# Optimization experiments

Measured on AMD Instinct MI355X. Metric: run time of the kernel, lower is better.

Reference implementation:

```python
import jax, jax.numpy as jnp
import numpy as np

D_MODEL = 2048
D_HEAD = 64
Q_HEADS = 32
KV_HEADS = 8


def rope(x):
    # x: [B, S, H, D], rotate interleaved pairs along last dim
    B, S, H, D = x.shape
    pos = jnp.arange(S, dtype=x.dtype)
    freq = 1.0 / (10000.0 ** (jnp.arange(0, D, 2, dtype=x.dtype) / D))  # [D/2]
    theta = pos[:, None] * freq[None, :]                                 # [S, D/2]
    cos = jnp.cos(theta)[None, :, None, :]
    sin = jnp.sin(theta)[None, :, None, :]
    xr = x.reshape(B, S, H, D // 2, 2)
    x1, x2 = xr[..., 0], xr[..., 1]
    out = jnp.stack((x1 * cos - x2 * sin, x1 * sin + x2 * cos), axis=-1)
    return out.reshape(B, S, H, D)


def setup_inputs() -> dict:
    key = jax.random.key(0)
    ks = jax.random.split(key, 7)
    x = jax.random.normal(ks[0], (1, 2048, D_MODEL), dtype=jnp.float32)
    W_q = jax.random.normal(ks[1], (Q_HEADS * D_HEAD, D_MODEL), dtype=jnp.float32) * 0.02
    b_q = jnp.zeros((Q_HEADS * D_HEAD,), dtype=jnp.float32)
    W_kv = jax.random.normal(ks[2], (2 * KV_HEADS * D_HEAD, D_MODEL), dtype=jnp.float32) * 0.02
    b_kv = jnp.zeros((2 * KV_HEADS * D_HEAD,), dtype=jnp.float32)
    W_out = jax.random.normal(ks[3], (D_MODEL, D_MODEL), dtype=jnp.float32) * 0.02
    b_out = jnp.zeros((D_MODEL,), dtype=jnp.float32)
    return {"x": x, "W_q": W_q, "b_q": b_q, "W_kv": W_kv, "b_kv": b_kv,
            "W_out": W_out, "b_out": b_out}


def reference(x, W_q, b_q, W_kv, b_kv, W_out, b_out):
    B, S, _ = x.shape
    g = Q_HEADS // KV_HEADS
    Q = (x @ W_q.T + b_q).reshape(B, S, Q_HEADS, D_HEAD)
    kv = x @ W_kv.T + b_kv
    K, V = jnp.split(kv, 2, axis=-1)
    K = K.reshape(B, S, KV_HEADS, D_HEAD)
    V = V.reshape(B, S, KV_HEADS, D_HEAD)
    Q = rope(Q)
    K = rope(K)
    K = jnp.repeat(K, g, axis=2)  # [B, S, Q_HEADS, D_HEAD]
    V = jnp.repeat(V, g, axis=2)
    scale = 1.0 / (D_HEAD ** 0.5)
    scores = jnp.einsum('bqhd,bkhd->bhqk', Q, K) * scale  # [B,H,S,S]
    # note: original calls non-inplace masked_fill and discards it, so no causal mask applied
    probs = jax.nn.softmax(scores, axis=-1)
    attn = jnp.einsum('bhqk,bkhd->bqhd', probs, V).reshape(B, S, D_MODEL)
    return attn @ W_out.T + b_out
```

## Files before the change

kernel.cpp:

```cpp
#include <hip/hip_runtime.h>
#include <hip/hip_bf16.h>
#include <math.h>

#define S_LEN 2048
#define D_MODEL 2048
#define Q_HEADS 32
#define KV_HEADS 8

typedef __attribute__((ext_vector_type(8))) short short8;
typedef __attribute__((ext_vector_type(4))) float f32x4;

__device__ __forceinline__ short bf16_rne(float f) {
  unsigned u = __float_as_uint(f);
  unsigned r = (u + 0x7FFFu + ((u >> 16) & 1u)) >> 16;
  return (short)r;
}
__device__ __forceinline__ void dma16(const short* g, short* l) {
  __builtin_amdgcn_global_load_lds(
      (const __attribute__((address_space(1))) void*)g,
      (__attribute__((address_space(3))) void*)l, 16, 0, 0);
}
__device__ __forceinline__ void fast_sincos(float theta, float& sn, float& cs) {
  double rev = (double)theta * 0.15915494309189535;
  float fr = (float)(rev - floor(rev));
  sn = __builtin_amdgcn_sinf(fr);
  cs = __builtin_amdgcn_cosf(fr);
}
__device__ __forceinline__ void cvt8(const float* src, short* dst, int i) {
  float4 a = *(const float4*)&src[i];
  float4 b = *(const float4*)&src[i + 4];
  short8 h;
  h[0] = bf16_rne(a.x); h[1] = bf16_rne(a.y);
  h[2] = bf16_rne(a.z); h[3] = bf16_rne(a.w);
  h[4] = bf16_rne(b.x); h[5] = bf16_rne(b.y);
  h[6] = bf16_rne(b.z); h[7] = bf16_rne(b.w);
  *(short8*)&dst[i] = h;
}

#define NM (2048 * 2048)
#define NKV (1024 * 2048)

__global__ __launch_bounds__(256) void cvt_all(
    const float* __restrict__ x,    short* __restrict__ xh,
    const float* __restrict__ wq,   short* __restrict__ wqh,
    const float* __restrict__ wkv,  short* __restrict__ wkvh,
    const float* __restrict__ wo,   short* __restrict__ woh) {
  int i = (blockIdx.x * 256 + threadIdx.x) * 8;
  if (i < NM) { cvt8(x, xh, i); return; }
  i -= NM;
  if (i < NM) { cvt8(wq, wqh, i); return; }
  i -= NM;
  if (i < NKV) { cvt8(wkv, wkvh, i); return; }
  i -= NKV;
  cvt8(wo, woh, i);
}

__global__ __launch_bounds__(256) void gemm_nt1_dual(
    const short* __restrict__ Ah,
    const short* __restrict__ Bq, const short* __restrict__ Bkv,
    const float* __restrict__ bq, const float* __restrict__ bkv,
    float* __restrict__ Cq, float* __restrict__ Ckv,
    int Nq, int Nkv, int K) {
  __shared__ short As[2][128 * 32];
  __shared__ short Bs[2][128 * 32];
  const int tid = threadIdx.x;
  const int w = tid >> 6, lane = tid & 63;
  const int l16 = lane & 15, quad = lane >> 4;
  const int bm = blockIdx.y * 128;
  const int bnG = blockIdx.x * 128;

  const short* Bsrc; const float* bias; float* Cp; int pitch; int bn;
  if (bnG < Nq) { Bsrc = Bq;  bias = bq;  Cp = Cq;  pitch = Nq;  bn = bnG; }
  else          { Bsrc = Bkv; bias = bkv; Cp = Ckv; pitch = Nkv; bn = bnG - Nq; }

  const int drow0 = w * 16 + (lane >> 2);
  const int drow1 = drow0 + 64;
  const int slot = lane & 3;
  const int ch0 = slot ^ ((drow0 >> 1) & 3);
  const int ch1 = slot ^ ((drow1 >> 1) & 3);
  const short* gA0 = &Ah[(size_t)(bm + drow0) * K + ch0 * 8];
  const short* gA1 = &Ah[(size_t)(bm + drow1) * K + ch1 * 8];
  const short* gB0 = &Bsrc[(size_t)(bn + drow0) * K + ch0 * 8];
  const short* gB1 = &Bsrc[(size_t)(bn + drow1) * K + ch1 * 8];
  const int dA0 = (w * 16) * 32, dA1 = (64 + w * 16) * 32;

  const int wm = (w & 1) * 64, wn = (w >> 1) * 64;
  int offA[4], offB[4];
#pragma unroll
  for (int i = 0; i < 4; ++i) {
    int R = wm + i * 16 + l16;
    offA[i] = R * 32 + (quad ^ ((R >> 1) & 3)) * 8;
    int Rb = wn + i * 16 + l16;
    offB[i] = Rb * 32 + (quad ^ ((Rb >> 1) & 3)) * 8;
  }

  f32x4 acc[4][4];
#pragma unroll
  for (int i = 0; i < 4; ++i)
#pragma unroll
    for (int j = 0; j < 4; ++j)
#pragma unroll
      for (int e = 0; e < 4; ++e) acc[i][j][e] = 0.f;

  const int T = K / 32;
  dma16(gA0, &As[0][dA0]);
  dma16(gA1, &As[0][dA1]);
  dma16(gB0, &Bs[0][dA0]);
  dma16(gB1, &Bs[0][dA1]);
  __syncthreads();

  for (int t = 0; t < T; ++t) {
    const int cur = t & 1, nxt = cur ^ 1;
    if (t + 1 < T) {
      const int ko = (t + 1) * 32;
      dma16(gA0 + ko, &As[nxt][dA0]);
      dma16(gA1 + ko, &As[nxt][dA1]);
      dma16(gB0 + ko, &Bs[nxt][dA0]);
      dma16(gB1 + ko, &Bs[nxt][dA1]);
    }
    short8 af[4], bf[4];
#pragma unroll
    for (int i = 0; i < 4; ++i) af[i] = *(const short8*)&As[cur][offA[i]];
#pragma unroll
    for (int j = 0; j < 4; ++j) bf[j] = *(const short8*)&Bs[cur][offB[j]];
#pragma unroll
    for (int i = 0; i < 4; ++i)
#pragma unroll
      for (int j = 0; j < 4; ++j)
        acc[i][j] = __builtin_amdgcn_mfma_f32_16x16x32_bf16(af[i], bf[j], acc[i][j], 0, 0, 0);
    __syncthreads();
  }

#pragma unroll
  for (int i = 0; i < 4; ++i) {
#pragma unroll
    for (int j = 0; j < 4; ++j) {
      const int col = bn + wn + j * 16 + l16;
      const float bv = bias[col];
      const int row0 = bm + wm + i * 16 + quad * 4;
#pragma unroll
      for (int e = 0; e < 4; ++e)
        Cp[(size_t)(row0 + e) * pitch + col] = acc[i][j][e] + bv;
    }
  }
}

__global__ __launch_bounds__(256) void gemm_nt1s(
    const short* __restrict__ A, const short* __restrict__ B,
    const float* __restrict__ bias, float* __restrict__ C,
    int N, int K) {
  __shared__ short As[2][128 * 32];
  __shared__ short Bs[2][64 * 32];
  const int tid = threadIdx.x;
  const int w = tid >> 6, lane = tid & 63;
  const int l16 = lane & 15, quad = lane >> 4;
  const int bm = blockIdx.y * 128;
  const int bn = blockIdx.x * 64;

  const int drow0 = w * 16 + (lane >> 2);
  const int drow1 = drow0 + 64;
  const int slot = lane & 3;
  const int ch0 = slot ^ ((drow0 >> 1) & 3);
  const int ch1 = slot ^ ((drow1 >> 1) & 3);
  const size_t a0 = (size_t)(bm + drow0) * K + ch0 * 8;
  const size_t a1 = (size_t)(bm + drow1) * K + ch1 * 8;
  const size_t b0 = (size_t)(bn + drow0) * K + ch0 * 8;
  const int dA0 = (w * 16) * 32, dA1 = (64 + w * 16) * 32;

  const int wm = (w & 1) * 64, wn = (w >> 1) * 32;
  int offA[4], offB[2];
#pragma unroll
  for (int i = 0; i < 4; ++i) {
    int R = wm + i * 16 + l16;
    offA[i] = R * 32 + (quad ^ ((R >> 1) & 3)) * 8;
  }
#pragma unroll
  for (int j = 0; j < 2; ++j) {
    int R = wn + j * 16 + l16;
    offB[j] = R * 32 + (quad ^ ((R >> 1) & 3)) * 8;
  }

  f32x4 acc[4][2];
#pragma unroll
  for (int i = 0; i < 4; ++i)
#pragma unroll
    for (int j = 0; j < 2; ++j)
#pragma unroll
      for (int e = 0; e < 4; ++e) acc[i][j][e] = 0.f;

  const int T = K / 32;
  dma16(A + a0, &As[0][dA0]);
  dma16(A + a1, &As[0][dA1]);
  dma16(B + b0, &Bs[0][dA0]);
  __syncthreads();

  for (int t = 0; t < T; ++t) {
    const int cur = t & 1, nxt = cur ^ 1;
    if (t + 1 < T) {
      const int ko = (t + 1) * 32;
      dma16(A + a0 + ko, &As[nxt][dA0]);
      dma16(A + a1 + ko, &As[nxt][dA1]);
      dma16(B + b0 + ko, &Bs[nxt][dA0]);
    }
    short8 af[4], bf[2];
#pragma unroll
    for (int i = 0; i < 4; ++i) af[i] = *(const short8*)&As[cur][offA[i]];
#pragma unroll
    for (int j = 0; j < 2; ++j) bf[j] = *(const short8*)&Bs[cur][offB[j]];
#pragma unroll
    for (int i = 0; i < 4; ++i)
#pragma unroll
      for (int j = 0; j < 2; ++j)
        acc[i][j] = __builtin_amdgcn_mfma_f32_16x16x32_bf16(af[i], bf[j], acc[i][j], 0, 0, 0);
    __syncthreads();
  }

#pragma unroll
  for (int i = 0; i < 4; ++i) {
#pragma unroll
    for (int j = 0; j < 2; ++j) {
      const int col = bn + wn + j * 16 + l16;
      const float bv = bias[col];
      const int row0 = bm + wm + i * 16 + quad * 4;
#pragma unroll
      for (int e = 0; e < 4; ++e)
        C[(size_t)(row0 + e) * N + col] = acc[i][j][e] + bv;
    }
  }
}

#define QSCALE 0.18033688011112042f

__global__ __launch_bounds__(256) void rope_q_pack(
    const float* __restrict__ Qf, short* __restrict__ Qb) {
  const int g = blockIdx.x * 256 + threadIdx.x;
  const int s = g >> 10;
  const int rem = g & 1023;
  const int h = rem >> 5, j = rem & 31;
  const double e = (2.0 * j) / 64.0;
  const float freq = (float)pow(10000.0, -e);
  const float theta = (float)s * freq;
  float sn, cs;
  fast_sincos(theta, sn, cs);
  const float* p = &Qf[(size_t)s * D_MODEL + h * 64 + 2 * j];
  const float x1 = p[0], x2 = p[1];
  short2 o;
  o.x = bf16_rne((x1 * cs - x2 * sn) * QSCALE);
  o.y = bf16_rne((x1 * sn + x2 * cs) * QSCALE);
  *(short2*)&Qb[((size_t)h * S_LEN + s) * 64 + 2 * j] = o;
}

__global__ __launch_bounds__(256) void rope_kv_pack(
    const float* __restrict__ KVf, short* __restrict__ Kb,
    short* __restrict__ Vt) {
  const int st = blockIdx.x, kvh = blockIdx.y;
  const int tid = threadIdx.x;
  __shared__ short Vtile[64][72];

  {
    const int sr = tid >> 2, sc = (tid & 3) * 16;
    const int s = st * 64 + sr;
    const float* kg = &KVf[(size_t)s * 1024 + kvh * 64 + sc];
    short tmp[16];
#pragma unroll
    for (int i = 0; i < 8; ++i) {
      const int j = (sc >> 1) + i;
      const double e = (2.0 * j) / 64.0;
      const float freq = (float)pow(10000.0, -e);
      const float theta = (float)s * freq;
      float sn, cs;
      fast_sincos(theta, sn, cs);
      const float x1 = kg[2 * i], x2 = kg[2 * i + 1];
      tmp[2 * i]     = bf16_rne(x1 * cs - x2 * sn);
      tmp[2 * i + 1] = bf16_rne(x1 * sn + x2 * cs);
    }
    short* out = &Kb[((size_t)kvh * S_LEN + s) * 64 + sc];
    *(short8*)&out[0] = *(short8*)&tmp[0];
    *(short8*)&out[8] = *(short8*)&tmp[8];
  }

  {
    const int sr = tid >> 2, sc = (tid & 3) * 16;
    const float* vg = &KVf[(size_t)(st * 64 + sr) * 1024 + 512 + kvh * 64 + sc];
    short tmp[16];
#pragma unroll
    for (int c = 0; c < 16; c += 4) {
      float4 v = *(const float4*)&vg[c];
      tmp[c + 0] = bf16_rne(v.x);
      tmp[c + 1] = bf16_rne(v.y);
      tmp[c + 2] = bf16_rne(v.z);
      tmp[c + 3] = bf16_rne(v.w);
    }
    *(short8*)&Vtile[sr][sc]     = *(short8*)&tmp[0];
    *(short8*)&Vtile[sr][sc + 8] = *(short8*)&tmp[8];
  }
  __syncthreads();
  {
    const int d = tid & 63, kchunk = tid >> 6;
    short tmp[16];
#pragma unroll
    for (int k = 0; k < 16; ++k) tmp[k] = Vtile[kchunk * 16 + k][d];
    short* out = &Vt[((size_t)kvh * 64 + d) * S_LEN + st * 64 + kchunk * 16];
    *(short8*)&out[0] = *(short8*)&tmp[0];
    *(short8*)&out[8] = *(short8*)&tmp[8];
  }
}

__global__ __launch_bounds__(256) void flash6(
    const short* __restrict__ Qb, const short* __restrict__ Kb,
    const short* __restrict__ Vt, short* __restrict__ Oh) {
  const int qt = blockIdx.x, h = blockIdx.y;
  const int kvh = h >> 2;
  const int tid = threadIdx.x;
  const int w = tid >> 6, lane = tid & 63;
  const int l16 = lane & 15, quad = lane >> 4;

  __shared__ short Ks[2][64 * 64];
  __shared__ short Vs[2][64 * 64];
  __shared__ short Ps[64 * 72];

  const short* Kh = Kb + (size_t)kvh * S_LEN * 64;
  const short* Vh = Vt + (size_t)kvh * 64 * S_LEN;
  const int qr = qt * 64 + w * 16 + l16;

  short8 qf0 = *(const short8*)&Qb[((size_t)h * S_LEN + qr) * 64 + quad * 8];
  short8 qf1 = *(const short8*)&Qb[((size_t)h * S_LEN + qr) * 64 + 32 + quad * 8];

  short8 ones;
#pragma unroll
  for (int e = 0; e < 8; ++e) ones[e] = (short)0x3F80;

  const int drow = lane >> 3;
  const int ch = (lane & 7) ^ drow;
  const short* gK = &Kh[(size_t)(w * 16 + drow) * 64 + ch * 8];
  const short* gV = &Vh[(size_t)(w * 16 + drow) * S_LEN + ch * 8];

  const int sl0 = quad ^ (l16 & 7);
  int offT[4][2];
#pragma unroll
  for (int m = 0; m < 4; ++m) {
    offT[m][0] = (m * 16 + l16) * 64 + sl0 * 8;
    offT[m][1] = (m * 16 + l16) * 64 + (sl0 ^ 4) * 8;
  }
  const int prow = (w * 16 + l16) * 72;

  f32x4 accl;
#pragma unroll
  for (int e = 0; e < 4; ++e) accl[e] = 0.f;
  f32x4 acco[4];
#pragma unroll
  for (int m = 0; m < 4; ++m)
#pragma unroll
    for (int e = 0; e < 4; ++e) acco[m][e] = 0.f;

  dma16(gK,               &Ks[0][(w * 16) * 64]);
  dma16(gK + 8 * 64,      &Ks[0][(w * 16 + 8) * 64]);
  dma16(gV,               &Vs[0][(w * 16) * 64]);
  dma16(gV + 8 * S_LEN,   &Vs[0][(w * 16 + 8) * 64]);
  __syncthreads();

  for (int t = 0; t < 32; ++t) {
    const int cur = t & 1, nxt = cur ^ 1;
    if (t + 1 < 32) {
      const short* gKn = gK + (t + 1) * 4096;
      const short* gVn = gV + (t + 1) * 64;
      dma16(gKn,             &Ks[nxt][(w * 16) * 64]);
      dma16(gKn + 8 * 64,    &Ks[nxt][(w * 16 + 8) * 64]);
      dma16(gVn,             &Vs[nxt][(w * 16) * 64]);
      dma16(gVn + 8 * S_LEN, &Vs[nxt][(w * 16 + 8) * 64]);
    }

    const short* kc = Ks[cur];
    f32x4 accs[4];
#pragma unroll
    for (int m = 0; m < 4; ++m)
#pragma unroll
      for (int e = 0; e < 4; ++e) accs[m][e] = 0.f;
#pragma unroll
    for (int m = 0; m < 4; ++m) {
      short8 k0 = *(const short8*)&kc[offT[m][0]];
      short8 k1 = *(const short8*)&kc[offT[m][1]];
      accs[m] = __builtin_amdgcn_mfma_f32_16x16x32_bf16(k0, qf0, accs[m], 0, 0, 0);
      accs[m] = __builtin_amdgcn_mfma_f32_16x16x32_bf16(k1, qf1, accs[m], 0, 0, 0);
    }

#pragma unroll
    for (int m = 0; m < 4; ++m) {
      float p0 = exp2f(accs[m][0]);
      float p1 = exp2f(accs[m][1]);
      float p2 = exp2f(accs[m][2]);
      float p3 = exp2f(accs[m][3]);
      unsigned u01 = __builtin_amdgcn_perm(__float_as_uint(p1), __float_as_uint(p0), 0x07060302u);
      unsigned u23 = __builtin_amdgcn_perm(__float_as_uint(p3), __float_as_uint(p2), 0x07060302u);
      *(uint2*)&Ps[prow + m * 16 + quad * 4] = make_uint2(u01, u23);
    }

    short8 pf0 = *(const short8*)&Ps[prow + quad * 8];
    short8 pf1 = *(const short8*)&Ps[prow + 32 + quad * 8];
    accl = __builtin_amdgcn_mfma_f32_16x16x32_bf16(ones, pf0, accl, 0, 0, 0);
    accl = __builtin_amdgcn_mfma_f32_16x16x32_bf16(ones, pf1, accl, 0, 0, 0);
    const short* vc = Vs[cur];
#pragma unroll
    for (int m = 0; m < 4; ++m) {
      short8 v0 = *(const short8*)&vc[offT[m][0]];
      short8 v1 = *(const short8*)&vc[offT[m][1]];
      acco[m] = __builtin_amdgcn_mfma_f32_16x16x32_bf16(v0, pf0, acco[m], 0, 0, 0);
      acco[m] = __builtin_amdgcn_mfma_f32_16x16x32_bf16(v1, pf1, acco[m], 0, 0, 0);
    }

    __syncthreads();
  }

  const float inv = 1.f / accl[0];
#pragma unroll
  for (int m = 0; m < 4; ++m) {
    short4 h4;
    h4.x = bf16_rne(acco[m][0] * inv);
    h4.y = bf16_rne(acco[m][1] * inv);
    h4.z = bf16_rne(acco[m][2] * inv);
    h4.w = bf16_rne(acco[m][3] * inv);
    const size_t base = (size_t)qr * D_MODEL + h * 64 + m * 16 + quad * 4;
    *(short4*)&Oh[base] = h4;
  }
}

extern "C" void kernel_launch(void* const* d_in, const int* in_sizes, int n_in,
                              void* d_out, int out_size, void* d_ws, size_t ws_size,
                              hipStream_t stream) {
  const float* x     = (const float*)d_in[0];
  const float* W_q   = (const float*)d_in[1];
  const float* b_q   = (const float*)d_in[2];
  const float* W_kv  = (const float*)d_in[3];
  const float* b_kv  = (const float*)d_in[4];
  const float* W_out = (const float*)d_in[5];
  const float* b_out = (const float*)d_in[6];
  float* out = (float*)d_out;

  char* ws = (char*)d_ws;
  float* Qbuf  = (float*)(ws);
  float* KVbuf = (float*)(ws + (16u << 20));
  short* xh    = (short*)(ws + (24u << 20));
  short* Wqh   = (short*)(ws + (32u << 20));
  short* Wkvh  = (short*)(ws + (40u << 20));
  short* Woh   = (short*)(ws + (44u << 20));
  short* Qb    = (short*)(ws + (52u << 20));
  short* Kb    = (short*)(ws + (60u << 20));
  short* Vtb   = (short*)(ws + (62u << 20));
  short* Ath   = xh;

  cvt_all<<<7168, 256, 0, stream>>>(x, xh, W_q, Wqh, W_kv, Wkvh, W_out, Woh);

  gemm_nt1_dual<<<dim3(3072 / 128, 2048 / 128), 256, 0, stream>>>(
      xh, Wqh, Wkvh, b_q, b_kv, Qbuf, KVbuf, 2048, 1024, 2048);

  rope_q_pack<<<(S_LEN * 1024) / 256, 256, 0, stream>>>(Qbuf, Qb);
  rope_kv_pack<<<dim3(S_LEN / 64, KV_HEADS), 256, 0, stream>>>(KVbuf, Kb, Vtb);

  flash6<<<dim3(S_LEN / 64, Q_HEADS), 256, 0, stream>>>(Qb, Kb, Vtb, Ath);

  gemm_nt1s<<<dim3(2048 / 64, 2048 / 128), 256, 0, stream>>>(
      Ath, Woh, b_out, out, 2048, 2048);
}
```

Measured before the change: 279.3 us.

## Load V fragments directly into registers in flash kernel; enlarge output GEMM tile

The attention kernel stops staging V through shared memory. Each wave now reads its V fragments straight from global memory into registers and prefetches the next tile after the PV MFMAs, which drops the V LDS buffers and cuts shared-memory use, and launch bounds now ask for four blocks per CU. The output projection GEMM moves from a 128x64 to a 128x128 tile so each block reuses the A tile across more columns, at the cost of fewer blocks (256) and more accumulator registers. Each wave redundantly loading the full V tile from global/L2 adds global traffic.

```diff
diff --git a/kernel.cpp b/kernel.cpp
--- a/kernel.cpp
+++ b/kernel.cpp
@@ -145,72 +145,72 @@
   }
 }
 
-__global__ __launch_bounds__(256) void gemm_nt1s(
+__global__ __launch_bounds__(256) void gemm_nt1_big(
     const short* __restrict__ A, const short* __restrict__ B,
     const float* __restrict__ bias, float* __restrict__ C,
     int N, int K) {
   __shared__ short As[2][128 * 32];
-  __shared__ short Bs[2][64 * 32];
+  __shared__ short Bs[2][128 * 32];
   const int tid = threadIdx.x;
   const int w = tid >> 6, lane = tid & 63;
   const int l16 = lane & 15, quad = lane >> 4;
   const int bm = blockIdx.y * 128;
-  const int bn = blockIdx.x * 64;
+  const int bn = blockIdx.x * 128;
 
   const int drow0 = w * 16 + (lane >> 2);
   const int drow1 = drow0 + 64;
   const int slot = lane & 3;
   const int ch0 = slot ^ ((drow0 >> 1) & 3);
   const int ch1 = slot ^ ((drow1 >> 1) & 3);
-  const size_t a0 = (size_t)(bm + drow0) * K + ch0 * 8;
-  const size_t a1 = (size_t)(bm + drow1) * K + ch1 * 8;
-  const size_t b0 = (size_t)(bn + drow0) * K + ch0 * 8;
+  const short* gA0 = &A[(size_t)(bm + drow0) * K + ch0 * 8];
+  const short* gA1 = &A[(size_t)(bm + drow1) * K + ch1 * 8];
+  const short* gB0 = &B[(size_t)(bn + drow0) * K + ch0 * 8];
+  const short* gB1 = &B[(size_t)(bn + drow1) * K + ch1 * 8];
   const int dA0 = (w * 16) * 32, dA1 = (64 + w * 16) * 32;
 
-  const int wm = (w & 1) * 64, wn = (w >> 1) * 32;
-  int offA[4], offB[2];
+  const int wm = (w & 1) * 64, wn = (w >> 1) * 64;
+  int offA[4], offB[4];
 #pragma unroll
   for (int i = 0; i < 4; ++i) {
     int R = wm + i * 16 + l16;
     offA[i] = R * 32 + (quad ^ ((R >> 1) & 3)) * 8;
-  }
-#pragma unroll
-  for (int j = 0; j < 2; ++j) {
-    int R = wn + j * 16 + l16;
-    offB[j] = R * 32 + (quad ^ ((R >> 1) & 3)) * 8;
-  }
-
-  f32x4 acc[4][2];
+    int Rb = wn + i * 16 + l16;
+    offB[i] = Rb * 32 + (quad ^ ((Rb >> 1) & 3)) * 8;
+  }
+
+  f32x4 acc[4][4];
 #pragma unroll
   for (int i = 0; i < 4; ++i)
 #pragma unroll
-    for (int j = 0; j < 2; ++j)
+    for (int j = 0; j < 4; ++j)
 #pragma unroll
       for (int e = 0; e < 4; ++e) acc[i][j][e] = 0.f;
 
   const int T = K / 32;
-  dma16(A + a0, &As[0][dA0]);
-  dma16(A + a1, &As[0][dA1]);
-  dma16(B + b0, &Bs[0][dA0]);
+  dma16(gA0, &As[0][dA0]);
+  dma16(gA1, &As[0][dA1]);
+  dma16(gB0, &Bs[0][dA0]);
+  dma16(gB1, &Bs[0][dA1]);
   __syncthreads();
 
   for (int t = 0; t < T; ++t) {
     const int cur = t & 1, nxt = cur ^ 1;
     if (t + 1 < T) {
       const int ko = (t + 1) * 32;
-      dma16(A + a0 + ko, &As[nxt][dA0]);
-      dma16(A + a1 + ko, &As[nxt][dA1]);
-      dma16(B + b0 + ko, &Bs[nxt][dA0]);
-    }
-    short8 af[4], bf[2];
+      dma16(gA0 + ko, &As[nxt][dA0]);
+      dma16(gA1 + ko, &As[nxt][dA1]);
+      dma16(gB0 + ko, &Bs[nxt][dA0]);
+      dma16(gB1 + ko, &Bs[nxt][dA1]);
+    }
+    short8 af[4], bf[4];
 #pragma unroll
     for (int i = 0; i < 4; ++i) af[i] = *(const short8*)&As[cur][offA[i]];
 #pragma unroll
-    for (int j = 0; j < 2; ++j) bf[j] = *(const short8*)&Bs[cur][offB[j]];
+    for (int j = 0; j < 4; ++j) bf[j] = *(const short8*)&Bs[cur][offB[j]];
 #pragma unroll
     for (int i = 0; i < 4; ++i)
 #pragma unroll
-      for (int j = 0; j < 2; ++j)
+      for (int j = 0; j < 4; ++j)
         acc[i][j] = __builtin_amdgcn_mfma_f32_16x16x32_bf16(af[i], bf[j], acc[i][j], 0, 0, 0);
     __syncthreads();
   }
@@ -218,7 +218,7 @@
 #pragma unroll
   for (int i = 0; i < 4; ++i) {
 #pragma unroll
-    for (int j = 0; j < 2; ++j) {
+    for (int j = 0; j < 4; ++j) {
       const int col = bn + wn + j * 16 + l16;
       const float bv = bias[col];
       const int row0 = bm + wm + i * 16 + quad * 4;
@@ -306,7 +306,7 @@
   }
 }
 
-__global__ __launch_bounds__(256) void flash6(
+__global__ __launch_bounds__(256, 4) void flash7(
     const short* __restrict__ Qb, const short* __restrict__ Kb,
     const short* __restrict__ Vt, short* __restrict__ Oh) {
   const int qt = blockIdx.x, h = blockIdx.y;
@@ -316,7 +316,6 @@
   const int l16 = lane & 15, quad = lane >> 4;
 
   __shared__ short Ks[2][64 * 64];
-  __shared__ short Vs[2][64 * 64];
   __shared__ short Ps[64 * 72];
 
   const short* Kh = Kb + (size_t)kvh * S_LEN * 64;
@@ -333,7 +332,6 @@
   const int drow = lane >> 3;
   const int ch = (lane & 7) ^ drow;
   const short* gK = &Kh[(size_t)(w * 16 + drow) * 64 + ch * 8];
-  const short* gV = &Vh[(size_t)(w * 16 + drow) * S_LEN + ch * 8];
 
   const int sl0 = quad ^ (l16 & 7);
   int offT[4][2];
@@ -344,6 +342,11 @@
   }
   const int prow = (w * 16 + l16) * 72;
 
+  const short* gV[4];
+#pragma unroll
+  for (int m = 0; m < 4; ++m)
+    gV[m] = &Vh[(size_t)(m * 16 + l16) * S_LEN + quad * 8];
+
   f32x4 accl;
 #pragma unroll
   for (int e = 0; e < 4; ++e) accl[e] = 0.f;
@@ -353,21 +356,22 @@
 #pragma unroll
     for (int e = 0; e < 4; ++e) acco[m][e] = 0.f;
 
-  dma16(gK,               &Ks[0][(w * 16) * 64]);
-  dma16(gK + 8 * 64,      &Ks[0][(w * 16 + 8) * 64]);
-  dma16(gV,               &Vs[0][(w * 16) * 64]);
-  dma16(gV + 8 * S_LEN,   &Vs[0][(w * 16 + 8) * 64]);
+  dma16(gK,          &Ks[0][(w * 16) * 64]);
+  dma16(gK + 8 * 64, &Ks[0][(w * 16 + 8) * 64]);
+  short8 vf[4][2];
+#pragma unroll
+  for (int m = 0; m < 4; ++m) {
+    vf[m][0] = *(const short8*)(gV[m]);
+    vf[m][1] = *(const short8*)(gV[m] + 32);
+  }
   __syncthreads();
 
   for (int t = 0; t < 32; ++t) {
     const int cur = t & 1, nxt = cur ^ 1;
     if (t + 1 < 32) {
       const short* gKn = gK + (t + 1) * 4096;
-      const short* gVn = gV + (t + 1) * 64;
-      dma16(gKn,             &Ks[nxt][(w * 16) * 64]);
-      dma16(gKn + 8 * 64,    &Ks[nxt][(w * 16 + 8) * 64]);
-      dma16(gVn,             &Vs[nxt][(w * 16) * 64]);
-      dma16(gVn + 8 * S_LEN, &Vs[nxt][(w * 16 + 8) * 64]);
+      dma16(gKn,          &Ks[nxt][(w * 16) * 64]);
+      dma16(gKn + 8 * 64, &Ks[nxt][(w * 16 + 8) * 64]);
     }
 
     const short* kc = Ks[cur];
@@ -399,13 +403,19 @@
     short8 pf1 = *(const short8*)&Ps[prow + 32 + quad * 8];
     accl = __builtin_amdgcn_mfma_f32_16x16x32_bf16(ones, pf0, accl, 0, 0, 0);
     accl = __builtin_amdgcn_mfma_f32_16x16x32_bf16(ones, pf1, accl, 0, 0, 0);
-    const short* vc = Vs[cur];
 #pragma unroll
     for (int m = 0; m < 4; ++m) {
-      short8 v0 = *(const short8*)&vc[offT[m][0]];
-      short8 v1 = *(const short8*)&vc[offT[m][1]];
-      acco[m] = __builtin_amdgcn_mfma_f32_16x16x32_bf16(v0, pf0, acco[m], 0, 0, 0);
-      acco[m] = __builtin_amdgcn_mfma_f32_16x16x32_bf16(v1, pf1, acco[m], 0, 0, 0);
+      acco[m] = __builtin_amdgcn_mfma_f32_16x16x32_bf16(vf[m][0], pf0, acco[m], 0, 0, 0);
+      acco[m] = __builtin_amdgcn_mfma_f32_16x16x32_bf16(vf[m][1], pf1, acco[m], 0, 0, 0);
+    }
+
+    if (t + 1 < 32) {
+      const int vo = (t + 1) * 64;
+#pragma unroll
+      for (int m = 0; m < 4; ++m) {
+        vf[m][0] = *(const short8*)(gV[m] + vo);
+        vf[m][1] = *(const short8*)(gV[m] + vo + 32);
+      }
     }
 
     __syncthreads();
@@ -456,8 +466,8 @@
   rope_q_pack<<<(S_LEN * 1024) / 256, 256, 0, stream>>>(Qbuf, Qb);
   rope_kv_pack<<<dim3(S_LEN / 64, KV_HEADS), 256, 0, stream>>>(KVbuf, Kb, Vtb);
 
-  flash6<<<dim3(S_LEN / 64, Q_HEADS), 256, 0, stream>>>(Qb, Kb, Vtb, Ath);
-
-  gemm_nt1s<<<dim3(2048 / 64, 2048 / 128), 256, 0, stream>>>(
+  flash7<<<dim3(S_LEN / 64, Q_HEADS), 256, 0, stream>>>(Qb, Kb, Vtb, Ath);
+
+  gemm_nt1_big<<<dim3(2048 / 128, 2048 / 128), 256, 0, stream>>>(
       Ath, Woh, b_out, out, 2048, 2048);
 }
```

After: 337.8 us. 20.9% more time.
